# Kernel optimization log

Hardware: AMD Instinct MI355X
Metric: run time of the kernel (lower is better)

The kernel has to match this reference:

```python
import math
import jax, jax.numpy as jnp
import numpy as np

DIM = 256
B, S = 4, 4096

def setup_inputs() -> dict:
    key = jax.random.key(0)
    k1, k2, k3 = jax.random.split(key, 3)
    X = jax.random.normal(k1, (B, S, DIM), dtype=jnp.float32)
    # torch nn.Linear(dim, 3*dim): weight [3*dim, dim], bias [3*dim]
    bound = 1.0 / math.sqrt(DIM)
    W = jax.random.uniform(k2, (3 * DIM, DIM), minval=-bound, maxval=bound, dtype=jnp.float32)
    b = jax.random.uniform(k3, (3 * DIM,), minval=-bound, maxval=bound, dtype=jnp.float32)
    return {"X": X, "W": W, "b": b}

def reference(X, W, b):
    # fused QKV projection: X @ W^T + b -> [B, S, 3*dim]
    QKV = jnp.einsum('bsd,ed->bse', X, W) + b
    Q, K, V = jnp.split(QKV, 3, axis=-1)
    # scaled dot-product attention (naive, full score matrix per original)
    scores = jnp.einsum('bqd,bkd->bqk', Q, K) / math.sqrt(DIM)
    att = jax.nn.softmax(scores, axis=-1)
    return jnp.einsum('bqk,bkd->bqd', att, V)
```

## Files before the change

### kernel.cpp

```cpp
#include <hip/hip_runtime.h>
#include <hip/hip_bf16.h>

#define B_ 4
#define S_ 4096
#define D_ 256

typedef __attribute__((ext_vector_type(8))) short bf16x8;
typedef __attribute__((ext_vector_type(4))) short short4v;
typedef __attribute__((ext_vector_type(4))) float f32x4;

static __device__ __forceinline__ unsigned short f2bf(float f) {
    unsigned int u = __float_as_uint(f);
    u += 0x7fffu + ((u >> 16) & 1u);
    return (unsigned short)(u >> 16);
}
static __device__ __forceinline__ float bf2f(unsigned short h) {
    return __uint_as_float(((unsigned int)h) << 16);
}
static __device__ __forceinline__ unsigned int cvtpk(float lo, float hi) {
    unsigned int r;
    asm("v_cvt_pk_bf16_f32 %0, %1, %2" : "=v"(r) : "v"(lo), "v"(hi));
    return r;
}

static __device__ __forceinline__ void gload16(const void* g, void* l) {
    __builtin_amdgcn_global_load_lds(
        (const __attribute__((address_space(1))) unsigned int*)g,
        (__attribute__((address_space(3))) unsigned int*)l, 16, 0, 0);
}

__global__ __launch_bounds__(256) void qkv_proj(
    const float* __restrict__ X, const float* __restrict__ W,
    const float* __restrict__ bias,
    unsigned short* __restrict__ Qb, unsigned short* __restrict__ Kb,
    unsigned short* __restrict__ Vt)
{
    __shared__ __align__(16) unsigned short As[64 * 64];
    __shared__ __align__(16) unsigned short Bs[64 * 64];

    const int tid  = threadIdx.x;
    const int lane = tid & 63;
    const int wid  = tid >> 6;
    const int wm   = wid >> 1, wn = wid & 1;
    const int c    = lane & 15, q4 = lane >> 4;
    const int gm0  = blockIdx.x * 64;
    const int gn0  = blockIdx.y * 64;
    const int sr   = tid >> 2;
    const int sc   = (tid & 3) * 16;

    f32x4 acc[2][2] = {};

    for (int kt = 0; kt < 4; ++kt) {
        const int k0 = kt * 64;
        {
            const float4* ga = (const float4*)(X + (size_t)(gm0 + sr) * D_ + k0 + sc);
            const float4* gb = (const float4*)(W + (size_t)(gn0 + sr) * D_ + k0 + sc);
            float4 a0 = ga[0], a1 = ga[1], a2 = ga[2], a3 = ga[3];
            float4 b0 = gb[0], b1 = gb[1], b2 = gb[2], b3 = gb[3];
            float af[16] = {a0.x,a0.y,a0.z,a0.w, a1.x,a1.y,a1.z,a1.w,
                            a2.x,a2.y,a2.z,a2.w, a3.x,a3.y,a3.z,a3.w};
            float bf[16] = {b0.x,b0.y,b0.z,b0.w, b1.x,b1.y,b1.z,b1.w,
                            b2.x,b2.y,b2.z,b2.w, b3.x,b3.y,b3.z,b3.w};
            bf16x8 av0, av1, bv0, bv1;
            #pragma unroll
            for (int j = 0; j < 8; ++j) {
                av0[j] = (short)f2bf(af[j]);     av1[j] = (short)f2bf(af[8 + j]);
                bv0[j] = (short)f2bf(bf[j]);     bv1[j] = (short)f2bf(bf[8 + j]);
            }
            const int sw = (sr & 7) << 3;
            *(bf16x8*)&As[sr * 64 + ((sc + 0) ^ sw)] = av0;
            *(bf16x8*)&As[sr * 64 + ((sc + 8) ^ sw)] = av1;
            *(bf16x8*)&Bs[sr * 64 + ((sc + 0) ^ sw)] = bv0;
            *(bf16x8*)&Bs[sr * 64 + ((sc + 8) ^ sw)] = bv1;
        }
        __syncthreads();
        const int sw = (c & 7) << 3;
        #pragma unroll
        for (int kk = 0; kk < 64; kk += 32) {
            bf16x8 afr[2], bfr[2];
            #pragma unroll
            for (int mf = 0; mf < 2; ++mf) {
                const int row = wm * 32 + mf * 16 + c;
                afr[mf] = *(const bf16x8*)&As[row * 64 + ((kk + 8 * q4) ^ sw)];
            }
            #pragma unroll
            for (int nf = 0; nf < 2; ++nf) {
                const int row = wn * 32 + nf * 16 + c;
                bfr[nf] = *(const bf16x8*)&Bs[row * 64 + ((kk + 8 * q4) ^ sw)];
            }
            #pragma unroll
            for (int mf = 0; mf < 2; ++mf)
                #pragma unroll
                for (int nf = 0; nf < 2; ++nf)
                    acc[mf][nf] = __builtin_amdgcn_mfma_f32_16x16x32_bf16(
                        afr[mf], bfr[nf], acc[mf][nf], 0, 0, 0);
        }
        __syncthreads();
    }

    const int b  = gm0 >> 12;
    const int s0 = gm0 & 4095;
    #pragma unroll
    for (int mf = 0; mf < 2; ++mf) {
        #pragma unroll
        for (int nf = 0; nf < 2; ++nf) {
            const int e  = gn0 + wn * 32 + nf * 16 + c;
            const float bv = bias[e];
            const int srow0 = s0 + wm * 32 + mf * 16 + 4 * q4;
            if (e < 256) {
                #pragma unroll
                for (int i = 0; i < 4; ++i)
                    Qb[((size_t)b * S_ + srow0 + i) * D_ + e] =
                        f2bf(acc[mf][nf][i] + bv);
            } else if (e < 512) {
                #pragma unroll
                for (int i = 0; i < 4; ++i)
                    Kb[((size_t)b * S_ + srow0 + i) * D_ + (e - 256)] =
                        f2bf(acc[mf][nf][i] + bv);
            } else {
                short4v pv;
                #pragma unroll
                for (int i = 0; i < 4; ++i)
                    pv[i] = (short)f2bf(acc[mf][nf][i] + bv);
                *(short4v*)&Vt[((size_t)(b * D_ + (e - 512))) * S_ + srow0] = pv;
            }
        }
    }
}

__global__ __launch_bounds__(512, 2) void attn_fwd(
    const unsigned short* __restrict__ Qb, const unsigned short* __restrict__ Kb,
    const unsigned short* __restrict__ Vt, float* __restrict__ Out)
{
    __shared__ __align__(16) char smem[132096];

    const int bid  = blockIdx.x;
    const int xcd  = bid & 7;
    const int tile = (xcd >> 1) * 64 + (bid >> 3) * 2 + (xcd & 1);
    const int gr0  = tile * 64;
    const int b    = gr0 >> 12;

    const int tid  = threadIdx.x;
    const int wid  = tid >> 6, lane = tid & 63;
    const int qi   = lane & 15, g = lane >> 4;
    const int rg   = wid & 3;
    const int kh   = wid >> 2;
    const int q0   = gr0 + rg * 16;
    const float C  = 0.09016844005556021f;
    const float THR = 40.0f;

    bf16x8 qf[8];
    {
        const size_t qrow = (size_t)(q0 + qi) * D_ + 8 * g;
        #pragma unroll
        for (int m = 0; m < 8; ++m)
            qf[m] = *(const bf16x8*)&Qb[qrow + m * 32];
    }

    const unsigned short* Kbb = Kb + (size_t)b * S_ * D_;
    const unsigned short* Vtb = Vt + (size_t)b * D_ * S_;

    const int isK = (wid < 4);
    const int sth = (wid >> 1) & 1;
    const int sub = wid & 1;
    int soff[8];
    int doff[8];
    if (isK) {
        const int l5 = lane >> 5, i5 = lane & 31;
        #pragma unroll
        for (int j = 0; j < 8; ++j) {
            const int r0 = sub * 16 + 2 * j + l5;
            soff[j] = (sth * 2048 + r0) * 256 + ((i5 ^ r0) << 3);
            doff[j] = sth * 16384 + (sub * 16 + 2 * j) * 512;
        }
    } else {
        #pragma unroll
        for (int j = 0; j < 8; ++j) {
            const int d = sub * 128 + 16 * j + (lane >> 2);
            soff[j] = d * S_ + sth * 2048 + ((((lane & 3) ^ ((lane >> 3) & 3))) << 3);
            doff[j] = 32768 + sth * 16384 + (sub * 128 + 16 * j) * 64;
        }
    }
    const unsigned short* sbase = isK ? Kbb : Vtb;

    float* Mbuf = (float*)(smem + 131072);
    float* Lbuf = (float*)(smem + 131584);

    f32x4 o[16] = {};
    float m0 = -1.0e30f, l0 = 0.0f;

    #pragma unroll
    for (int j = 0; j < 8; ++j)
        gload16(sbase + soff[j], smem + doff[j]);
    __builtin_amdgcn_s_waitcnt(0);
    __syncthreads();

    const int NS = 64;
    int p = 0;
    const int vsw = (g ^ ((qi >> 1) & 3)) << 4;

    for (int s = 0; s < NS; ++s) {
        if (s + 1 < NS) {
            const unsigned short* sb = sbase + (isK ? (s + 1) * 32 * 256
                                                    : (s + 1) * 32);
            const int bufo = (p ^ 1) * 65536;
            #pragma unroll
            for (int j = 0; j < 8; ++j)
                gload16(sb + soff[j], smem + bufo + doff[j]);
        }

        const char* Ksb = smem + p * 65536 + kh * 16384;
        const char* Vsb = smem + p * 65536 + 32768 + kh * 16384;

        f32x4 sacc[2] = {};
        #pragma unroll
        for (int kc = 0; kc < 2; ++kc) {
            const int kr = kc * 16 + qi;
            const char* krow = Ksb + kr * 512;
            #pragma unroll
            for (int m = 0; m < 8; ++m) {
                bf16x8 kf = *(const bf16x8*)(krow + (((4 * m + g) ^ kr) << 4));
                sacc[kc] = __builtin_amdgcn_mfma_f32_16x16x32_bf16(
                    kf, qf[m], sacc[kc], 0, 0, 0);
            }
        }

        float rmax = fmaxf(fmaxf(fmaxf(sacc[0][0], sacc[0][1]),
                                 fmaxf(sacc[0][2], sacc[0][3])),
                           fmaxf(fmaxf(sacc[1][0], sacc[1][1]),
                                 fmaxf(sacc[1][2], sacc[1][3])));
        rmax = fmaxf(rmax, __shfl_xor(rmax, 16));
        rmax = fmaxf(rmax, __shfl_xor(rmax, 32));

        if (__any(rmax > m0 + THR)) {
            const float mn = fmaxf(m0, rmax);
            const float corr = exp2f((m0 - mn) * C);
            m0 = mn;
            l0 *= corr;
            #pragma unroll
            for (int dc = 0; dc < 16; ++dc)
                #pragma unroll
                for (int r = 0; r < 4; ++r) o[dc][r] *= corr;
        }

        float p8[2][4];
        float rsum = 0.f;
        #pragma unroll
        for (int kc = 0; kc < 2; ++kc)
            #pragma unroll
            for (int r = 0; r < 4; ++r) {
                p8[kc][r] = exp2f((sacc[kc][r] - m0) * C);
                rsum += p8[kc][r];
            }
        rsum += __shfl_xor(rsum, 16);
        rsum += __shfl_xor(rsum, 32);
        l0 += rsum;

        unsigned int pk0[2], pk1[2];
        pk0[0] = cvtpk(p8[0][0], p8[0][1]);  pk0[1] = cvtpk(p8[0][2], p8[0][3]);
        pk1[0] = cvtpk(p8[1][0], p8[1][1]);  pk1[1] = cvtpk(p8[1][2], p8[1][3]);

        const int A0 = qi + ((g & 1) << 5);
        const int A1 = A0 + 16;
        const unsigned int s00 = __shfl(pk0[0], A0), s01 = __shfl(pk0[1], A0);
        const unsigned int s02 = __shfl(pk0[0], A1), s03 = __shfl(pk0[1], A1);
        const unsigned int s10 = __shfl(pk1[0], A0), s11 = __shfl(pk1[1], A0);
        const unsigned int s12 = __shfl(pk1[0], A1), s13 = __shfl(pk1[1], A1);
        const bool hk = (g >> 1);
        union U { unsigned int w[4]; bf16x8 v; } pa;
        pa.w[0] = hk ? s10 : s00;  pa.w[1] = hk ? s11 : s01;
        pa.w[2] = hk ? s12 : s02;  pa.w[3] = hk ? s13 : s03;

        #pragma unroll
        for (int dc = 0; dc < 16; ++dc) {
            bf16x8 vf = *(const bf16x8*)(Vsb + (dc * 16 + qi) * 64 + vsw);
            o[dc] = __builtin_amdgcn_mfma_f32_16x16x32_bf16(vf, pa.v, o[dc], 0, 0, 0);
        }

        __syncthreads();
        p ^= 1;
    }

    const int qidx = rg * 16 + qi;
    if (g == 0) Mbuf[qidx * 2 + kh] = m0;
    __syncthreads();

    {
        const float gm = fmaxf(Mbuf[qidx * 2], Mbuf[qidx * 2 + 1]);
        const float corr = exp2f((m0 - gm) * C);
        l0 *= corr;
        #pragma unroll
        for (int dc = 0; dc < 16; ++dc)
            #pragma unroll
            for (int r = 0; r < 4; ++r) o[dc][r] *= corr;
    }
    if (g == 0) Lbuf[qidx * 2 + kh] = l0;

    float* Obuf = (float*)smem;
    if (kh == 1) {
        #pragma unroll
        for (int dc = 0; dc < 16; ++dc)
            #pragma unroll
            for (int r = 0; r < 4; ++r)
                Obuf[qidx * 260 + dc * 16 + 4 * g + r] = o[dc][r];
    }
    __syncthreads();

    if (kh == 0) {
        const float inv = 1.0f / (Lbuf[qidx * 2] + Lbuf[qidx * 2 + 1]);
        #pragma unroll
        for (int dc = 0; dc < 16; ++dc)
            #pragma unroll
            for (int r = 0; r < 4; ++r) {
                const int d = dc * 16 + 4 * g + r;
                Out[(size_t)(q0 + qi) * D_ + d] =
                    (o[dc][r] + Obuf[qidx * 260 + d]) * inv;
            }
    }
}

extern "C" void kernel_launch(void* const* d_in, const int* in_sizes, int n_in,
                              void* d_out, int out_size, void* d_ws, size_t ws_size,
                              hipStream_t stream) {
    (void)out_size; (void)ws_size;
    const void *Xp = nullptr, *Wp = nullptr, *bp = nullptr;
    for (int i = 0; i < n_in; ++i) {
        if      (in_sizes[i] == B_ * S_ * D_) Xp = d_in[i];
        else if (in_sizes[i] == 3 * D_ * D_)  Wp = d_in[i];
        else if (in_sizes[i] == 3 * D_)       bp = d_in[i];
    }
    if (!Xp) Xp = d_in[0];
    if (!Wp) Wp = d_in[1];
    if (!bp) bp = d_in[2];

    float* Out = (float*)d_out;

    unsigned short* Qb = (unsigned short*)d_ws;
    unsigned short* Kb = Qb + (size_t)B_ * S_ * D_;
    unsigned short* Vt = Kb + (size_t)B_ * S_ * D_;

    dim3 pgrid(256, 12);
    qkv_proj<<<pgrid, 256, 0, stream>>>((const float*)Xp, (const float*)Wp,
                                        (const float*)bp, Qb, Kb, Vt);
    attn_fwd<<<256, 512, 0, stream>>>(Qb, Kb, Vt, Out);
}
```

Baseline: 161.8 us.

## Share K/V fragments across two query tiles per wave with four-way key split

Each wave now processes 32 query rows (two 16-row tiles) against a 16-key slice, so every K and V fragment read from LDS feeds two MFMAs. The key dimension is split four ways across waves instead of two, the P·V product switches to 16x16x16 MFMA to avoid the cross-lane shuffle repacking of probabilities, and s_setprio is raised around the MFMA bursts. The cost is double the accumulator registers (two 256-wide output tiles per wave), more work in the final reduction across the four key-split partials, and a larger LDS footprint.

```diff
diff --git a/kernel.cpp b/kernel.cpp
--- a/kernel.cpp
+++ b/kernel.cpp
@@ -28,6 +28,19 @@
         (const __attribute__((address_space(1))) unsigned int*)g,
         (__attribute__((address_space(3))) unsigned int*)l, 16, 0, 0);
 }
+
+#if __has_builtin(__builtin_amdgcn_mfma_f32_16x16x16bf16_1k)
+#define MFMA16(a, b, c) __builtin_amdgcn_mfma_f32_16x16x16bf16_1k(a, b, c, 0, 0, 0)
+#elif __has_builtin(__builtin_amdgcn_mfma_f32_16x16x16_bf16)
+#define MFMA16(a, b, c) __builtin_amdgcn_mfma_f32_16x16x16_bf16(a, b, c, 0, 0, 0)
+#else
+static __device__ __forceinline__ f32x4 mfma16_asm(short4v a, short4v b, f32x4 c) {
+    asm volatile("v_mfma_f32_16x16x16_bf16 %0, %1, %2, %0"
+                 : "+v"(c) : "v"(a), "v"(b));
+    return c;
+}
+#define MFMA16(a, b, c) mfma16_asm(a, b, c)
+#endif
 
 __global__ __launch_bounds__(256) void qkv_proj(
     const float* __restrict__ X, const float* __restrict__ W,
@@ -132,7 +145,7 @@
     const unsigned short* __restrict__ Qb, const unsigned short* __restrict__ Kb,
     const unsigned short* __restrict__ Vt, float* __restrict__ Out)
 {
-    __shared__ __align__(16) char smem[132096];
+    __shared__ __align__(16) char smem[135680];
 
     const int bid  = blockIdx.x;
     const int xcd  = bid & 7;
@@ -143,51 +156,49 @@
     const int tid  = threadIdx.x;
     const int wid  = tid >> 6, lane = tid & 63;
     const int qi   = lane & 15, g = lane >> 4;
-    const int rg   = wid & 3;
-    const int kh   = wid >> 2;
-    const int q0   = gr0 + rg * 16;
+    const int rg   = wid & 1;
+    const int kq   = wid >> 1;
+    const int q0   = gr0 + rg * 32;
     const float C  = 0.09016844005556021f;
     const float THR = 40.0f;
 
-    bf16x8 qf[8];
+    bf16x8 qfa[8], qfb[8];
     {
-        const size_t qrow = (size_t)(q0 + qi) * D_ + 8 * g;
-        #pragma unroll
-        for (int m = 0; m < 8; ++m)
-            qf[m] = *(const bf16x8*)&Qb[qrow + m * 32];
+        const size_t qra = (size_t)(q0 + qi) * D_ + 8 * g;
+        const size_t qrb = (size_t)(q0 + 16 + qi) * D_ + 8 * g;
+        #pragma unroll
+        for (int m = 0; m < 8; ++m) {
+            qfa[m] = *(const bf16x8*)&Qb[qra + m * 32];
+            qfb[m] = *(const bf16x8*)&Qb[qrb + m * 32];
+        }
     }
 
     const unsigned short* Kbb = Kb + (size_t)b * S_ * D_;
     const unsigned short* Vtb = Vt + (size_t)b * D_ * S_;
 
     const int isK = (wid < 4);
-    const int sth = (wid >> 1) & 1;
-    const int sub = wid & 1;
-    int soff[8];
-    int doff[8];
+    const int sq  = isK ? wid : wid - 4;
+    int soff[8], doff[8];
     if (isK) {
-        const int l5 = lane >> 5, i5 = lane & 31;
         #pragma unroll
         for (int j = 0; j < 8; ++j) {
-            const int r0 = sub * 16 + 2 * j + l5;
-            soff[j] = (sth * 2048 + r0) * 256 + ((i5 ^ r0) << 3);
-            doff[j] = sth * 16384 + (sub * 16 + 2 * j) * 512;
+            const int r0 = 2 * j + (lane >> 5);
+            soff[j] = (sq * 1024 + r0) * 256 + (((lane & 31) ^ r0) << 3);
+            doff[j] = sq * 8192 + j * 1024;
         }
     } else {
         #pragma unroll
         for (int j = 0; j < 8; ++j) {
-            const int d = sub * 128 + 16 * j + (lane >> 2);
-            soff[j] = d * S_ + sth * 2048 + ((((lane & 3) ^ ((lane >> 3) & 3))) << 3);
-            doff[j] = 32768 + sth * 16384 + (sub * 128 + 16 * j) * 64;
+            const int d = 32 * j + (lane >> 1);
+            soff[j] = d * S_ + sq * 1024 +
+                      (((lane & 1) ^ ((lane >> 3) & 1)) << 3);
+            doff[j] = 32768 + sq * 8192 + j * 1024;
         }
     }
     const unsigned short* sbase = isK ? Kbb : Vtb;
 
-    float* Mbuf = (float*)(smem + 131072);
-    float* Lbuf = (float*)(smem + 131584);
-
-    f32x4 o[16] = {};
-    float m0 = -1.0e30f, l0 = 0.0f;
+    f32x4 oA[16] = {}, oB[16] = {};
+    float m0a = -1.0e30f, l0a = 0.0f, m0b = -1.0e30f, l0b = 0.0f;
 
     #pragma unroll
     for (int j = 0; j < 8; ++j)
@@ -197,124 +208,166 @@
 
     const int NS = 64;
     int p = 0;
-    const int vsw = (g ^ ((qi >> 1) & 3)) << 4;
+    const int vbyte = (((g >> 1) ^ ((qi >> 2) & 1)) << 4) + ((g & 1) << 3);
 
     for (int s = 0; s < NS; ++s) {
         if (s + 1 < NS) {
-            const unsigned short* sb = sbase + (isK ? (s + 1) * 32 * 256
-                                                    : (s + 1) * 32);
+            const unsigned short* sb = sbase + (isK ? (s + 1) * 4096
+                                                    : (s + 1) * 16);
             const int bufo = (p ^ 1) * 65536;
             #pragma unroll
             for (int j = 0; j < 8; ++j)
                 gload16(sb + soff[j], smem + bufo + doff[j]);
         }
 
-        const char* Ksb = smem + p * 65536 + kh * 16384;
-        const char* Vsb = smem + p * 65536 + 32768 + kh * 16384;
-
-        f32x4 sacc[2] = {};
-        #pragma unroll
-        for (int kc = 0; kc < 2; ++kc) {
-            const int kr = kc * 16 + qi;
-            const char* krow = Ksb + kr * 512;
-            #pragma unroll
-            for (int m = 0; m < 8; ++m) {
-                bf16x8 kf = *(const bf16x8*)(krow + (((4 * m + g) ^ kr) << 4));
-                sacc[kc] = __builtin_amdgcn_mfma_f32_16x16x32_bf16(
-                    kf, qf[m], sacc[kc], 0, 0, 0);
-            }
-        }
-
-        float rmax = fmaxf(fmaxf(fmaxf(sacc[0][0], sacc[0][1]),
-                                 fmaxf(sacc[0][2], sacc[0][3])),
-                           fmaxf(fmaxf(sacc[1][0], sacc[1][1]),
-                                 fmaxf(sacc[1][2], sacc[1][3])));
-        rmax = fmaxf(rmax, __shfl_xor(rmax, 16));
-        rmax = fmaxf(rmax, __shfl_xor(rmax, 32));
-
-        if (__any(rmax > m0 + THR)) {
-            const float mn = fmaxf(m0, rmax);
-            const float corr = exp2f((m0 - mn) * C);
-            m0 = mn;
-            l0 *= corr;
+        const char* Ksb = smem + p * 65536 + kq * 8192;
+        const char* Vsb = smem + p * 65536 + 32768 + kq * 8192;
+
+        f32x4 sa = {}, sb2 = {};
+        __builtin_amdgcn_s_setprio(1);
+        #pragma unroll
+        for (int m = 0; m < 8; ++m) {
+            bf16x8 kf = *(const bf16x8*)(Ksb + qi * 512 +
+                                         ((((m << 2) + g) ^ qi) << 4));
+            sa  = __builtin_amdgcn_mfma_f32_16x16x32_bf16(kf, qfa[m], sa, 0, 0, 0);
+            sb2 = __builtin_amdgcn_mfma_f32_16x16x32_bf16(kf, qfb[m], sb2, 0, 0, 0);
+        }
+        __builtin_amdgcn_s_setprio(0);
+
+        float ra = fmaxf(fmaxf(sa[0], sa[1]), fmaxf(sa[2], sa[3]));
+        float rb = fmaxf(fmaxf(sb2[0], sb2[1]), fmaxf(sb2[2], sb2[3]));
+        ra = fmaxf(ra, __shfl_xor(ra, 16));  ra = fmaxf(ra, __shfl_xor(ra, 32));
+        rb = fmaxf(rb, __shfl_xor(rb, 16));  rb = fmaxf(rb, __shfl_xor(rb, 32));
+
+        if (__any((ra > m0a + THR) || (rb > m0b + THR))) {
+            const float mna = fmaxf(m0a, ra), mnb = fmaxf(m0b, rb);
+            const float ca = exp2f((m0a - mna) * C);
+            const float cb = exp2f((m0b - mnb) * C);
+            m0a = mna; l0a *= ca;  m0b = mnb; l0b *= cb;
             #pragma unroll
             for (int dc = 0; dc < 16; ++dc)
                 #pragma unroll
-                for (int r = 0; r < 4; ++r) o[dc][r] *= corr;
-        }
-
-        float p8[2][4];
-        float rsum = 0.f;
-        #pragma unroll
-        for (int kc = 0; kc < 2; ++kc)
-            #pragma unroll
-            for (int r = 0; r < 4; ++r) {
-                p8[kc][r] = exp2f((sacc[kc][r] - m0) * C);
-                rsum += p8[kc][r];
-            }
-        rsum += __shfl_xor(rsum, 16);
-        rsum += __shfl_xor(rsum, 32);
-        l0 += rsum;
-
-        unsigned int pk0[2], pk1[2];
-        pk0[0] = cvtpk(p8[0][0], p8[0][1]);  pk0[1] = cvtpk(p8[0][2], p8[0][3]);
-        pk1[0] = cvtpk(p8[1][0], p8[1][1]);  pk1[1] = cvtpk(p8[1][2], p8[1][3]);
-
-        const int A0 = qi + ((g & 1) << 5);
-        const int A1 = A0 + 16;
-        const unsigned int s00 = __shfl(pk0[0], A0), s01 = __shfl(pk0[1], A0);
-        const unsigned int s02 = __shfl(pk0[0], A1), s03 = __shfl(pk0[1], A1);
-        const unsigned int s10 = __shfl(pk1[0], A0), s11 = __shfl(pk1[1], A0);
-        const unsigned int s12 = __shfl(pk1[0], A1), s13 = __shfl(pk1[1], A1);
-        const bool hk = (g >> 1);
-        union U { unsigned int w[4]; bf16x8 v; } pa;
-        pa.w[0] = hk ? s10 : s00;  pa.w[1] = hk ? s11 : s01;
-        pa.w[2] = hk ? s12 : s02;  pa.w[3] = hk ? s13 : s03;
-
+                for (int r = 0; r < 4; ++r) {
+                    oA[dc][r] *= ca;  oB[dc][r] *= cb;
+                }
+        }
+
+        float pa[4], pb[4];
+        float rsa = 0.f, rsb = 0.f;
+        #pragma unroll
+        for (int r = 0; r < 4; ++r) {
+            pa[r] = exp2f((sa[r]  - m0a) * C);  rsa += pa[r];
+            pb[r] = exp2f((sb2[r] - m0b) * C);  rsb += pb[r];
+        }
+        rsa += __shfl_xor(rsa, 16);  rsa += __shfl_xor(rsa, 32);  l0a += rsa;
+        rsb += __shfl_xor(rsb, 16);  rsb += __shfl_xor(rsb, 32);  l0b += rsb;
+
+        union U { unsigned int w[2]; short4v v; } ua, ub;
+        ua.w[0] = cvtpk(pa[0], pa[1]);  ua.w[1] = cvtpk(pa[2], pa[3]);
+        ub.w[0] = cvtpk(pb[0], pb[1]);  ub.w[1] = cvtpk(pb[2], pb[3]);
+
+        __builtin_amdgcn_s_setprio(1);
         #pragma unroll
         for (int dc = 0; dc < 16; ++dc) {
-            bf16x8 vf = *(const bf16x8*)(Vsb + (dc * 16 + qi) * 64 + vsw);
-            o[dc] = __builtin_amdgcn_mfma_f32_16x16x32_bf16(vf, pa.v, o[dc], 0, 0, 0);
-        }
+            short4v vf = *(const short4v*)(Vsb + (dc * 16 + qi) * 32 + vbyte);
+            oA[dc] = MFMA16(vf, ua.v, oA[dc]);
+            oB[dc] = MFMA16(vf, ub.v, oB[dc]);
+        }
+        __builtin_amdgcn_s_setprio(0);
 
         __syncthreads();
         p ^= 1;
     }
 
-    const int qidx = rg * 16 + qi;
-    if (g == 0) Mbuf[qidx * 2 + kh] = m0;
+    float* Mbuf = (float*)(smem + 133632);
+    float* Lbuf = (float*)(smem + 134656);
+    const int rowA = rg * 32 + qi, rowB = rowA + 16;
+
+    if (g == 0) { Mbuf[rowA * 4 + kq] = m0a;  Mbuf[rowB * 4 + kq] = m0b; }
     __syncthreads();
 
     {
-        const float gm = fmaxf(Mbuf[qidx * 2], Mbuf[qidx * 2 + 1]);
-        const float corr = exp2f((m0 - gm) * C);
-        l0 *= corr;
-        #pragma unroll
-        for (int dc = 0; dc < 16; ++dc)
-            #pragma unroll
-            for (int r = 0; r < 4; ++r) o[dc][r] *= corr;
-    }
-    if (g == 0) Lbuf[qidx * 2 + kh] = l0;
-
-    float* Obuf = (float*)smem;
-    if (kh == 1) {
-        #pragma unroll
-        for (int dc = 0; dc < 16; ++dc)
-            #pragma unroll
-            for (int r = 0; r < 4; ++r)
-                Obuf[qidx * 260 + dc * 16 + 4 * g + r] = o[dc][r];
-    }
-    __syncthreads();
-
-    if (kh == 0) {
-        const float inv = 1.0f / (Lbuf[qidx * 2] + Lbuf[qidx * 2 + 1]);
-        #pragma unroll
-        for (int dc = 0; dc < 16; ++dc)
-            #pragma unroll
-            for (int r = 0; r < 4; ++r) {
-                const int d = dc * 16 + 4 * g + r;
-                Out[(size_t)(q0 + qi) * D_ + d] =
-                    (o[dc][r] + Obuf[qidx * 260 + d]) * inv;
+        const float* ma = &Mbuf[rowA * 4];
+        const float* mb = &Mbuf[rowB * 4];
+        const float gma = fmaxf(fmaxf(ma[0], ma[1]), fmaxf(ma[2], ma[3]));
+        const float gmb = fmaxf(fmaxf(mb[0], mb[1]), fmaxf(mb[2], mb[3]));
+        const float ca = exp2f((m0a - gma) * C);
+        const float cb = exp2f((m0b - gmb) * C);
+        l0a *= ca;  l0b *= cb;
+        #pragma unroll
+        for (int dc = 0; dc < 16; ++dc)
+            #pragma unroll
+            for (int r = 0; r < 4; ++r) {
+                oA[dc][r] *= ca;  oB[dc][r] *= cb;
+            }
+    }
+    if (g == 0) { Lbuf[rowA * 4 + kq] = l0a;  Lbuf[rowB * 4 + kq] = l0b; }
+    __syncthreads();
+
+    const float* la = &Lbuf[rowA * 4];
+    const float* lb = &Lbuf[rowB * 4];
+    const float invA = 1.0f / (la[0] + la[1] + la[2] + la[3]);
+    const float invB = 1.0f / (lb[0] + lb[1] + lb[2] + lb[3]);
+
+    float* R1 = (float*)smem;
+    float* R3 = (float*)(smem + 66816);
+
+    if (kq == 1 || kq == 3) {
+        float* R = (kq == 1) ? R1 : R3;
+        #pragma unroll
+        for (int dc = 0; dc < 16; ++dc)
+            #pragma unroll
+            for (int r = 0; r < 4; ++r) {
+                const int col = dc * 16 + 4 * g + r;
+                R[rowA * 261 + col] = oA[dc][r];
+                R[rowB * 261 + col] = oB[dc][r];
+            }
+    }
+    __syncthreads();
+
+    if (kq == 0) {
+        #pragma unroll
+        for (int dc = 0; dc < 16; ++dc)
+            #pragma unroll
+            for (int r = 0; r < 4; ++r) {
+                const int col = dc * 16 + 4 * g + r;
+                oA[dc][r] += R1[rowA * 261 + col];
+                oB[dc][r] += R1[rowB * 261 + col];
+            }
+    }
+    if (kq == 2) {
+        #pragma unroll
+        for (int dc = 0; dc < 16; ++dc)
+            #pragma unroll
+            for (int r = 0; r < 4; ++r) {
+                const int col = dc * 16 + 4 * g + r;
+                oA[dc][r] += R3[rowA * 261 + col];
+                oB[dc][r] += R3[rowB * 261 + col];
+            }
+    }
+    __syncthreads();
+    if (kq == 2) {
+        #pragma unroll
+        for (int dc = 0; dc < 16; ++dc)
+            #pragma unroll
+            for (int r = 0; r < 4; ++r) {
+                const int col = dc * 16 + 4 * g + r;
+                R3[rowA * 261 + col] = oA[dc][r];
+                R3[rowB * 261 + col] = oB[dc][r];
+            }
+    }
+    __syncthreads();
+
+    if (kq == 0) {
+        #pragma unroll
+        for (int dc = 0; dc < 16; ++dc)
+            #pragma unroll
+            for (int r = 0; r < 4; ++r) {
+                const int col = dc * 16 + 4 * g + r;
+                Out[(size_t)(q0 + qi) * D_ + col] =
+                    (oA[dc][r] + R3[rowA * 261 + col]) * invA;
+                Out[(size_t)(q0 + 16 + qi) * D_ + col] =
+                    (oB[dc][r] + R3[rowB * 261 + col]) * invB;
             }
     }
 }
```

Measured after the change: 234.3 us. 1.45x slower.
